# Kernel optimization log

Hardware: AMD Instinct MI355X
Metric: run time of the kernel (lower is better)

Reference implementation:

```python
import jax, jax.numpy as jnp
from jax import lax
import numpy as np

B, S_DEC, S_ENC = 32, 128, 128
V, E, H = 32000, 200, 128


def setup_inputs() -> dict:
    key = jax.random.key(0)
    ks = jax.random.split(key, 10)
    emb = jax.random.normal(ks[0], (V, E), dtype=jnp.float32)
    emb = emb.at[0].set(0.0)  # padding_idx row (char2id[' '] -> 0)
    return {
        "sequence": jax.random.randint(ks[1], (B, S_DEC), 0, V),
        "hs": jax.random.normal(ks[2], (B, S_ENC, H), dtype=jnp.float32),
        "h": jax.random.normal(ks[3], (1, B, H), dtype=jnp.float32),
        "emb": emb,
        "w_ih": jax.random.normal(ks[4], (3 * H, E), dtype=jnp.float32) * 0.05,
        "w_hh": jax.random.normal(ks[5], (3 * H, H), dtype=jnp.float32) * 0.05,
        "b_ih": jax.random.normal(ks[6], (3 * H,), dtype=jnp.float32) * 0.05,
        "b_hh": jax.random.normal(ks[7], (3 * H,), dtype=jnp.float32) * 0.05,
        "w_out": jax.random.normal(ks[8], (V, 2 * H), dtype=jnp.float32) * 0.05,
        "b_out": jax.random.normal(ks[9], (V,), dtype=jnp.float32) * 0.05,
    }


def _gru(x_gates, h0, w_hh, b_hh):
    # x_gates: [B, S, 3H] precomputed input projections; torch gate order r,z,n
    def step(hprev, xg):
        hg = hprev @ w_hh.T + b_hh
        xr, xz, xn = jnp.split(xg, 3, axis=-1)
        hr, hz, hn = jnp.split(hg, 3, axis=-1)
        r = jax.nn.sigmoid(xr + hr)
        z = jax.nn.sigmoid(xz + hz)
        n = jnp.tanh(xn + r * hn)
        hnew = (1.0 - z) * n + z * hprev
        return hnew, hnew

    hT, outs = lax.scan(step, h0, jnp.swapaxes(x_gates, 0, 1))  # scan over time
    return jnp.swapaxes(outs, 0, 1), hT  # [B,S,H], [B,H]


def reference(sequence, hs, h, emb, w_ih, w_hh, b_ih, b_hh, w_out, b_out):
    # Embedding lookup (padding row already zero)
    x = emb[sequence]  # [B, S_dec, E]
    x_gates = jnp.einsum("bse,ge->bsg", x, w_ih) + b_ih  # [B, S_dec, 3H]
    output, hT = _gru(x_gates, h[0], w_hh, b_hh)  # [B, S_dec, H]
    state = hT[None]  # [1, B, H]
    # s = bmm(hs, output^T): [B, S_enc, S_dec]; softmax over encoder axis (dim=1)
    s = jnp.einsum("beh,bdh->bed", hs, output)
    attention_weight = jax.nn.softmax(s, axis=1)
    # context: replaces the per-timestep python loop with one contraction
    c = jnp.einsum("bed,beh->bdh", attention_weight, hs)  # [B, S_dec, H]
    cat = jnp.concatenate([output, c], axis=-1)  # [B, S_dec, 2H]
    logits = jnp.einsum("bdh,vh->bdv", cat, w_out) + b_out  # [B, S_dec, V]
    return logits, state, attention_weight
```

## Files before the change

### kernel.cpp

```cpp
#include <hip/hip_runtime.h>
#include <hip/hip_bf16.h>

#define B_    32
#define SDEC  128
#define SENC  128
#define V_    32000
#define E_    200
#define H_    128
#define G3    384

typedef __attribute__((ext_vector_type(8))) short bf16x8;
typedef __attribute__((ext_vector_type(4))) float f32x4;
typedef __attribute__((ext_vector_type(2))) float f32x2;

#define GLOBAL_AS __attribute__((address_space(1)))
#define LDS_AS    __attribute__((address_space(3)))

__device__ __forceinline__ float fast_sigmoid(float x) {
  return 1.f / (1.f + __expf(-x));
}
__device__ __forceinline__ float fast_tanh(float x) {
  float e2 = __expf(2.f * x);
  return 1.f - 2.f / (e2 + 1.f);
}
__device__ __forceinline__ float quad_reduce(float x) {
  int i = __builtin_bit_cast(int, x);
  int a = __builtin_amdgcn_mov_dpp(i, 0xB1, 0xF, 0xF, true);
  float s = x + __builtin_bit_cast(float, a);
  int j = __builtin_bit_cast(int, s);
  int c = __builtin_amdgcn_mov_dpp(j, 0x4E, 0xF, 0xF, true);
  return s + __builtin_bit_cast(float, c);
}

__global__ __launch_bounds__(192) void k_embed_proj(
    const int* __restrict__ seq, const float* __restrict__ emb,
    const float* __restrict__ w_ih, const float* __restrict__ b_ih,
    float* __restrict__ xg) {
  __shared__ __align__(16) float xs[16][E_];
  __shared__ int sidx[16];
  const int r0 = blockIdx.x * 16;
  const int t = threadIdx.x;
  if (t < 16) sidx[t] = seq[r0 + t];
  __syncthreads();
  for (int i = t; i < 800; i += 192) {
    int r = i / 50, c = i - r * 50;
    *(float4*)&xs[r][c * 4] =
        *(const float4*)(emb + (size_t)sidx[r] * E_ + c * 4);
  }
  __syncthreads();
  const int g0 = t, g1 = t + 192;
  float a0[16], a1[16];
#pragma unroll
  for (int r = 0; r < 16; r++) { a0[r] = 0.f; a1[r] = 0.f; }
  const float* w0 = w_ih + (size_t)g0 * E_;
  const float* w1 = w_ih + (size_t)g1 * E_;
  for (int k = 0; k < E_; k += 4) {
    float4 wv0 = *(const float4*)(w0 + k);
    float4 wv1 = *(const float4*)(w1 + k);
#pragma unroll
    for (int r = 0; r < 16; r++) {
      float4 xv = *(const float4*)&xs[r][k];
      a0[r] += wv0.x * xv.x + wv0.y * xv.y + wv0.z * xv.z + wv0.w * xv.w;
      a1[r] += wv1.x * xv.x + wv1.y * xv.y + wv1.z * xv.z + wv1.w * xv.w;
    }
  }
  const float b0 = b_ih[g0], b1 = b_ih[g1];
#pragma unroll
  for (int r = 0; r < 16; r++) {
    xg[(size_t)(r0 + r) * G3 + g0] = a0[r] + b0;
    xg[(size_t)(r0 + r) * G3 + g1] = a1[r] + b1;
  }
}

__global__ __launch_bounds__(512) void k_gru_attn_cvt(
    const float* __restrict__ xg, const float* __restrict__ h0,
    const float* __restrict__ w_hh, const float* __restrict__ b_hh,
    const float* __restrict__ hs, __hip_bfloat16* __restrict__ cat_bf,
    float* __restrict__ state_out, float* __restrict__ attw_out,
    const float* __restrict__ w_out, __hip_bfloat16* __restrict__ wout_bf) {
  if (blockIdx.x >= 32) {
    const int base = (blockIdx.x - 32) * 4;
#pragma unroll
    for (int j = 0; j < 4; j++) {
      int idx = ((base + j) * 512 + threadIdx.x) * 8;
      float4 a = *(const float4*)(w_out + idx);
      float4 c = *(const float4*)(w_out + idx + 4);
      union { __hip_bfloat16 h[8]; uint4 v; } p;
      p.h[0] = __float2bfloat16(a.x); p.h[1] = __float2bfloat16(a.y);
      p.h[2] = __float2bfloat16(a.z); p.h[3] = __float2bfloat16(a.w);
      p.h[4] = __float2bfloat16(c.x); p.h[5] = __float2bfloat16(c.y);
      p.h[6] = __float2bfloat16(c.z); p.h[7] = __float2bfloat16(c.w);
      *(uint4*)(wout_bf + idx) = p.v;
    }
    return;
  }

  __shared__ __hip_bfloat16 ctb[128][128];
  __shared__ __hip_bfloat16 hsb[128][128];
  __shared__ __hip_bfloat16 hsT[128][128];
  __shared__ __align__(16) float hp[2][H_];

  const int b = blockIdx.x;
  const int t = threadIdx.x;
  const int hh = t >> 2;
  const int sub = t & 3;

  float wr_[32], wz_[32], wn_[32];
#pragma unroll
  for (int m = 0; m < 8; m++) {
    int c = (m + sub * 2) & 7;
    int kb = sub * 32 + c * 4;
    *(float4*)&wr_[m * 4] = *(const float4*)(w_hh + (size_t)hh * H_ + kb);
    *(float4*)&wz_[m * 4] = *(const float4*)(w_hh + (size_t)(128 + hh) * H_ + kb);
    *(float4*)&wn_[m * 4] = *(const float4*)(w_hh + (size_t)(256 + hh) * H_ + kb);
  }

  const float* xgb = xg + (size_t)b * SDEC * G3;
  const float br = b_hh[hh], bz = b_hh[128 + hh], bn = b_hh[256 + hh];
  float cxr = xgb[hh], cxz = xgb[128 + hh], cxn = xgb[256 + hh];
  if (t < H_) hp[0][t] = h0[b * H_ + t];
  __hip_bfloat16* catbfb = cat_bf + (size_t)b * SDEC * 256;

  asm volatile("s_waitcnt lgkmcnt(0)" ::: "memory");
  __builtin_amdgcn_s_barrier();
  asm volatile("" ::: "memory");

  int cur = 0;
  for (int s = 0; s < SDEC; s++) {
    float nxr = 0.f, nxz = 0.f, nxn = 0.f;
    if (s + 1 < SDEC) {
      const float* xp = xgb + (size_t)(s + 1) * G3;
      nxr = xp[hh]; nxz = xp[128 + hh]; nxn = xp[256 + hh];
    }
    f32x2 sr2 = {0.f, 0.f}, sz2 = {0.f, 0.f}, sn2 = {0.f, 0.f};
#pragma unroll
    for (int m = 0; m < 8; m++) {
      int c = (m + sub * 2) & 7;
      float4 hv = *(const float4*)&hp[cur][sub * 32 + c * 4];
      f32x2 h01 = {hv.x, hv.y}, h23 = {hv.z, hv.w};
      const f32x2* w2r = (const f32x2*)&wr_[m * 4];
      const f32x2* w2z = (const f32x2*)&wz_[m * 4];
      const f32x2* w2n = (const f32x2*)&wn_[m * 4];
      sr2 += w2r[0] * h01; sr2 += w2r[1] * h23;
      sz2 += w2z[0] * h01; sz2 += w2z[1] * h23;
      sn2 += w2n[0] * h01; sn2 += w2n[1] * h23;
    }
    float sr = quad_reduce(sr2[0] + sr2[1]);
    float sz = quad_reduce(sz2[0] + sz2[1]);
    float sn = quad_reduce(sn2[0] + sn2[1]);

    float hold = hp[cur][hh];
    float r = fast_sigmoid(cxr + sr + br);
    float z = fast_sigmoid(cxz + sz + bz);
    float n = fast_tanh(cxn + r * (sn + bn));
    float hnew = (1.f - z) * n + z * hold;
    if (sub == 0) {
      __hip_bfloat16 hb = __float2bfloat16(hnew);
      hp[cur ^ 1][hh] = hnew;
      catbfb[(size_t)s * 256 + hh] = hb;
      ctb[s][((hh >> 3) ^ (s & 7)) * 8 + (hh & 7)] = hb;
    }
    asm volatile("s_waitcnt lgkmcnt(0)" ::: "memory");
    __builtin_amdgcn_s_barrier();
    asm volatile("" ::: "memory");
    cur ^= 1;
    cxr = nxr; cxz = nxz; cxn = nxn;
  }

  const int w = t >> 6, l = t & 63;
  const int lr = l & 15, lk = l >> 4;
  const float* hsbase = hs + (size_t)b * SENC * H_;

  for (int i = t; i < 2048; i += 512) {
    int e = i >> 4, c = i & 15;
    float4 v0 = *(const float4*)(hsbase + e * H_ + c * 8);
    float4 v1 = *(const float4*)(hsbase + e * H_ + c * 8 + 4);
    union { __hip_bfloat16 h[8]; uint4 u; } pk;
    pk.h[0] = __float2bfloat16(v0.x); pk.h[1] = __float2bfloat16(v0.y);
    pk.h[2] = __float2bfloat16(v0.z); pk.h[3] = __float2bfloat16(v0.w);
    pk.h[4] = __float2bfloat16(v1.x); pk.h[5] = __float2bfloat16(v1.y);
    pk.h[6] = __float2bfloat16(v1.z); pk.h[7] = __float2bfloat16(v1.w);
    *(uint4*)&hsb[e][((c ^ (e & 7)) * 8)] = pk.u;
  }
  if (t < H_) state_out[b * H_ + t] = hp[cur][t];
  __syncthreads();

  for (int i = t; i < 2048; i += 512) {
    int c = i >> 7, e = i & 127;
    uint4 v = *(const uint4*)&hsb[e][((c ^ (e & 7)) * 8)];
    const __hip_bfloat16* hv = (const __hip_bfloat16*)&v;
#pragma unroll
    for (int u = 0; u < 8; u++) {
      int h = c * 8 + u;
      int col = (e + 8 * (h & 15)) & 127;
      hsT[h][col] = hv[u];
    }
  }
  const int d = w * 16 + lr;
  bf16x8 afrag[4];
#pragma unroll
  for (int kt = 0; kt < 4; kt++)
    afrag[kt] = *(const bf16x8*)&ctb[d][(((kt * 4 + lk) ^ (lr & 7)) * 8)];
  __syncthreads();

  f32x4 acc[8];
#pragma unroll
  for (int et = 0; et < 8; et++) acc[et] = (f32x4){0.f, 0.f, 0.f, 0.f};
#pragma unroll
  for (int et = 0; et < 8; et++) {
#pragma unroll
    for (int kt = 0; kt < 4; kt++) {
      bf16x8 bfrag =
          *(const bf16x8*)&hsb[et * 16 + lr][(((kt * 4 + lk) ^ (lr & 7)) * 8)];
      acc[et] =
          __builtin_amdgcn_mfma_f32_16x16x32_bf16(bfrag, afrag[kt], acc[et], 0, 0, 0);
    }
  }

  float mx = -1e30f;
#pragma unroll
  for (int et = 0; et < 8; et++)
    mx = fmaxf(mx, fmaxf(fmaxf(acc[et][0], acc[et][1]),
                         fmaxf(acc[et][2], acc[et][3])));
  mx = fmaxf(mx, __shfl_xor(mx, 16));
  mx = fmaxf(mx, __shfl_xor(mx, 32));
  float sum = 0.f;
#pragma unroll
  for (int et = 0; et < 8; et++) {
    acc[et][0] = __expf(acc[et][0] - mx);
    acc[et][1] = __expf(acc[et][1] - mx);
    acc[et][2] = __expf(acc[et][2] - mx);
    acc[et][3] = __expf(acc[et][3] - mx);
    sum += acc[et][0] + acc[et][1] + acc[et][2] + acc[et][3];
  }
  sum += __shfl_xor(sum, 16);
  sum += __shfl_xor(sum, 32);
  const float inv = 1.f / sum;

  __hip_bfloat16 (*plds)[128] = ctb;
  float* aw = attw_out + (size_t)b * SENC * SDEC + d;
#pragma unroll
  for (int et = 0; et < 8; et++) {
    acc[et][0] *= inv; acc[et][1] *= inv;
    acc[et][2] *= inv; acc[et][3] *= inv;
    union { __hip_bfloat16 h[4]; uint2 u; } pk4;
    pk4.h[0] = __float2bfloat16(acc[et][0]);
    pk4.h[1] = __float2bfloat16(acc[et][1]);
    pk4.h[2] = __float2bfloat16(acc[et][2]);
    pk4.h[3] = __float2bfloat16(acc[et][3]);
    *(uint2*)&plds[d][(((et * 2 + (lk >> 1)) ^ (lr & 7)) * 8 + 4 * (lk & 1))] =
        pk4.u;
    const int e0 = et * 16 + lk * 4;
#pragma unroll
    for (int j = 0; j < 4; j++)
      aw[(size_t)(e0 + j) * SDEC] = acc[et][j];
  }
  __syncthreads();

  bf16x8 pfrag[4];
#pragma unroll
  for (int f = 0; f < 4; f++)
    pfrag[f] = *(const bf16x8*)&plds[d][(((f * 4 + lk) ^ (lr & 7)) * 8)];
#pragma unroll
  for (int ht = 0; ht < 8; ht++) {
    f32x4 a2 = (f32x4){0.f, 0.f, 0.f, 0.f};
#pragma unroll
    for (int kt = 0; kt < 4; kt++) {
      bf16x8 hfrag =
          *(const bf16x8*)&hsT[ht * 16 + lr][((kt * 32 + lk * 8 + 8 * lr) & 127)];
      a2 = __builtin_amdgcn_mfma_f32_16x16x32_bf16(hfrag, pfrag[kt], a2, 0, 0, 0);
    }
    union { __hip_bfloat16 h[4]; uint2 u; } pk4;
    pk4.h[0] = __float2bfloat16(a2[0]);
    pk4.h[1] = __float2bfloat16(a2[1]);
    pk4.h[2] = __float2bfloat16(a2[2]);
    pk4.h[3] = __float2bfloat16(a2[3]);
    *(uint2*)(cat_bf + (size_t)(b * SDEC + d) * 256 + 128 + ht * 16 + lk * 4) =
        pk4.u;
  }
}

__global__ __launch_bounds__(512) void k_gemm_mfma(
    const __hip_bfloat16* __restrict__ A, const __hip_bfloat16* __restrict__ Bw,
    const float* __restrict__ b_out, float* __restrict__ C) {
  constexpr int K = 256, N = V_, Kt = 32;
  alignas(16) __shared__ char smem[49152];
  __hip_bfloat16 (*As)[4096] = (__hip_bfloat16(*)[4096])smem;
  __hip_bfloat16 (*Bs)[8192] = (__hip_bfloat16(*)[8192])(smem + 16384);
  float* tr = (float*)smem;

  const int tid = threadIdx.x;
  const int w = tid >> 6, l = tid & 63;
  const int wr = w >> 2, wc = w & 3;
  const int lr = l & 15, lk = l >> 4;
  const int lq = l >> 2, lc = l & 3;

  const int bid = blockIdx.x;
  const int wgid = (bid & 7) * 500 + (bid >> 3);
  const int mt = wgid & 31;
  const int nt = wgid >> 5;
  const int m0 = mt * 128, n0 = nt * 256;

  f32x4 acc[4][4];
#pragma unroll
  for (int m = 0; m < 4; m++)
#pragma unroll
    for (int n = 0; n < 4; n++) acc[m][n] = (f32x4){0.f, 0.f, 0.f, 0.f};

#define STAGE(buf, kk)                                                            \
  do {                                                                            \
    const __hip_bfloat16* gA = A + (size_t)(m0 + w * 16 + lq) * K + (kk) + lc * 8;\
    const __hip_bfloat16* gB0 = Bw + (size_t)(n0 + w * 32 + lq) * K + (kk) + lc * 8;\
    const __hip_bfloat16* gB1 = gB0 + (size_t)16 * K;                             \
    __builtin_amdgcn_global_load_lds((const GLOBAL_AS void*)gA,                   \
        (LDS_AS void*)(&As[buf][w * 512]), 16, 0, 0);                             \
    __builtin_amdgcn_global_load_lds((const GLOBAL_AS void*)gB0,                  \
        (LDS_AS void*)(&Bs[buf][w * 1024]), 16, 0, 0);                            \
    __builtin_amdgcn_global_load_lds((const GLOBAL_AS void*)gB1,                  \
        (LDS_AS void*)(&Bs[buf][w * 1024 + 512]), 16, 0, 0);                      \
  } while (0)

  STAGE(0, 0);
  STAGE(1, Kt);

#pragma unroll
  for (int t = 0; t < 8; ++t) {
    if (t < 7) asm volatile("s_waitcnt vmcnt(3)" ::: "memory");
    else       asm volatile("s_waitcnt vmcnt(0)" ::: "memory");
    __builtin_amdgcn_s_barrier();
    asm volatile("" ::: "memory");

    const int c = t & 1;
    bf16x8 af[4], bfr[4];
#pragma unroll
    for (int m = 0; m < 4; m++)
      af[m] = *(const bf16x8*)(const void*)(&As[c][(wr * 64 + m * 16 + lr) * Kt + lk * 8]);
#pragma unroll
    for (int n = 0; n < 4; n++)
      bfr[n] = *(const bf16x8*)(const void*)(&Bs[c][(wc * 64 + n * 16 + lr) * Kt + lk * 8]);

    asm volatile("s_waitcnt lgkmcnt(0)" ::: "memory");
    __builtin_amdgcn_s_barrier();
    asm volatile("" ::: "memory");

    if (t < 6) STAGE(c, (t + 2) * Kt);

    __builtin_amdgcn_s_setprio(1);
#pragma unroll
    for (int m = 0; m < 4; m++)
#pragma unroll
      for (int n = 0; n < 4; n++)
        acc[m][n] = __builtin_amdgcn_mfma_f32_16x16x32_bf16(bfr[n], af[m], acc[m][n], 0, 0, 0);
    __builtin_amdgcn_s_setprio(0);
  }
#undef STAGE

  float4 bo_n[4];
#pragma unroll
  for (int n = 0; n < 4; n++)
    bo_n[n] = *(const float4*)(b_out + n0 + wc * 64 + n * 16 + lk * 4);

  __syncthreads();
#pragma unroll
  for (int q = 0; q < 4; ++q) {
    if (wr == (q >> 1)) {
      const int mbase = 2 * (q & 1);
#pragma unroll
      for (int mm = 0; mm < 2; mm++) {
        const int m = mbase + mm;
        const int row = mm * 16 + lr;
#pragma unroll
        for (int n = 0; n < 4; n++) {
          const int col = wc * 64 + n * 16 + lk * 4;
          f32x4 v;
          v[0] = acc[m][n][0] + bo_n[n].x;
          v[1] = acc[m][n][1] + bo_n[n].y;
          v[2] = acc[m][n][2] + bo_n[n].z;
          v[3] = acc[m][n][3] + bo_n[n].w;
          *(f32x4*)&tr[row * 260 + col] = v;
        }
      }
    }
    __syncthreads();
#pragma unroll
    for (int i = 0; i < 4; ++i) {
      const int c2 = i * 512 + tid;
      const int row = c2 >> 6;
      const int off = (c2 & 63) * 4;
      f32x4 v = *(const f32x4*)&tr[row * 260 + off];
      __builtin_nontemporal_store(
          v, (f32x4*)(C + (size_t)(m0 + q * 32 + row) * N + n0 + off));
    }
    __syncthreads();
  }
}

extern "C" void kernel_launch(void* const* d_in, const int* in_sizes, int n_in,
                              void* d_out, int out_size, void* d_ws, size_t ws_size,
                              hipStream_t stream) {
  const int* seq = (const int*)d_in[0];
  const float* hs = (const float*)d_in[1];
  const float* h0 = (const float*)d_in[2];
  const float* emb = (const float*)d_in[3];
  const float* w_ih = (const float*)d_in[4];
  const float* w_hh = (const float*)d_in[5];
  const float* b_ih = (const float*)d_in[6];
  const float* b_hh = (const float*)d_in[7];
  const float* w_out = (const float*)d_in[8];
  const float* b_out = (const float*)d_in[9];

  float* out = (float*)d_out;
  float* logits = out;
  float* state = out + 131072000;
  float* attw = out + 131072000 + 4096;

  char* ws = (char*)d_ws;
  float* xg = (float*)ws;
  __hip_bfloat16* cat_bf = (__hip_bfloat16*)(ws + 10485760);
  __hip_bfloat16* wout_bf = (__hip_bfloat16*)(ws + 12582912);

  k_embed_proj<<<256, 192, 0, stream>>>(seq, emb, w_ih, b_ih, xg);
  k_gru_attn_cvt<<<532, 512, 0, stream>>>(xg, h0, w_hh, b_hh, hs, cat_bf,
                                          state, attw, w_out, wout_bf);
  k_gemm_mfma<<<4000, 512, 0, stream>>>(cat_bf, wout_bf, b_out, logits);
}
```

Before: 292.3 us.

## Enlarge GEMM M-tile to 256 with triple-buffered LDS and fewer barriers

The logits GEMM now computes 256x256 output tiles per workgroup, so the grid halves and each B tile loaded from global memory is reused across twice as many rows. Staging moves to a three-slot LDS ring, which drops the second per-iteration barrier and the s_setprio hints; A fragments are loaded per m-row inside the MFMA loop. The epilogue writes 64 rows per pass. Separately, the embedding projection kernel uses 128 threads, each computing three gate columns instead of two. The cost is 96KB of LDS and more accumulator registers per workgroup, which limits occupancy to one workgroup per CU.

```diff
diff --git a/kernel.cpp b/kernel.cpp
--- a/kernel.cpp
+++ b/kernel.cpp
@@ -32,7 +32,7 @@
   return s + __builtin_bit_cast(float, c);
 }
 
-__global__ __launch_bounds__(192) void k_embed_proj(
+__global__ __launch_bounds__(128) void k_embed_proj(
     const int* __restrict__ seq, const float* __restrict__ emb,
     const float* __restrict__ w_ih, const float* __restrict__ b_ih,
     float* __restrict__ xg) {
@@ -42,33 +42,37 @@
   const int t = threadIdx.x;
   if (t < 16) sidx[t] = seq[r0 + t];
   __syncthreads();
-  for (int i = t; i < 800; i += 192) {
+  for (int i = t; i < 800; i += 128) {
     int r = i / 50, c = i - r * 50;
     *(float4*)&xs[r][c * 4] =
         *(const float4*)(emb + (size_t)sidx[r] * E_ + c * 4);
   }
   __syncthreads();
-  const int g0 = t, g1 = t + 192;
-  float a0[16], a1[16];
-#pragma unroll
-  for (int r = 0; r < 16; r++) { a0[r] = 0.f; a1[r] = 0.f; }
+  const int g0 = t, g1 = t + 128, g2 = t + 256;
+  float a0[16], a1[16], a2[16];
+#pragma unroll
+  for (int r = 0; r < 16; r++) { a0[r] = 0.f; a1[r] = 0.f; a2[r] = 0.f; }
   const float* w0 = w_ih + (size_t)g0 * E_;
   const float* w1 = w_ih + (size_t)g1 * E_;
+  const float* w2 = w_ih + (size_t)g2 * E_;
   for (int k = 0; k < E_; k += 4) {
     float4 wv0 = *(const float4*)(w0 + k);
     float4 wv1 = *(const float4*)(w1 + k);
+    float4 wv2 = *(const float4*)(w2 + k);
 #pragma unroll
     for (int r = 0; r < 16; r++) {
       float4 xv = *(const float4*)&xs[r][k];
       a0[r] += wv0.x * xv.x + wv0.y * xv.y + wv0.z * xv.z + wv0.w * xv.w;
       a1[r] += wv1.x * xv.x + wv1.y * xv.y + wv1.z * xv.z + wv1.w * xv.w;
-    }
-  }
-  const float b0 = b_ih[g0], b1 = b_ih[g1];
+      a2[r] += wv2.x * xv.x + wv2.y * xv.y + wv2.z * xv.z + wv2.w * xv.w;
+    }
+  }
+  const float b0 = b_ih[g0], b1 = b_ih[g1], b2 = b_ih[g2];
 #pragma unroll
   for (int r = 0; r < 16; r++) {
     xg[(size_t)(r0 + r) * G3 + g0] = a0[r] + b0;
     xg[(size_t)(r0 + r) * G3 + g1] = a1[r] + b1;
+    xg[(size_t)(r0 + r) * G3 + g2] = a2[r] + b2;
   }
 }
 
@@ -280,13 +284,13 @@
   }
 }
 
-__global__ __launch_bounds__(512) void k_gemm_mfma(
+__global__ __launch_bounds__(512, 2) void k_gemm_mfma(
     const __hip_bfloat16* __restrict__ A, const __hip_bfloat16* __restrict__ Bw,
     const float* __restrict__ b_out, float* __restrict__ C) {
   constexpr int K = 256, N = V_, Kt = 32;
-  alignas(16) __shared__ char smem[49152];
-  __hip_bfloat16 (*As)[4096] = (__hip_bfloat16(*)[4096])smem;
-  __hip_bfloat16 (*Bs)[8192] = (__hip_bfloat16(*)[8192])(smem + 16384);
+  alignas(16) __shared__ char smem[98304];
+  __hip_bfloat16 (*As)[8192] = (__hip_bfloat16(*)[8192])smem;
+  __hip_bfloat16 (*Bs)[8192] = (__hip_bfloat16(*)[8192])(smem + 49152);
   float* tr = (float*)smem;
 
   const int tid = threadIdx.x;
@@ -296,24 +300,27 @@
   const int lq = l >> 2, lc = l & 3;
 
   const int bid = blockIdx.x;
-  const int wgid = (bid & 7) * 500 + (bid >> 3);
-  const int mt = wgid & 31;
-  const int nt = wgid >> 5;
-  const int m0 = mt * 128, n0 = nt * 256;
-
-  f32x4 acc[4][4];
-#pragma unroll
-  for (int m = 0; m < 4; m++)
+  const int wgid = (bid & 7) * 250 + (bid >> 3);
+  const int mt = wgid & 15;
+  const int nt = wgid >> 4;
+  const int m0 = mt * 256, n0 = nt * 256;
+
+  f32x4 acc[8][4];
+#pragma unroll
+  for (int m = 0; m < 8; m++)
 #pragma unroll
     for (int n = 0; n < 4; n++) acc[m][n] = (f32x4){0.f, 0.f, 0.f, 0.f};
 
 #define STAGE(buf, kk)                                                            \
   do {                                                                            \
-    const __hip_bfloat16* gA = A + (size_t)(m0 + w * 16 + lq) * K + (kk) + lc * 8;\
+    const __hip_bfloat16* gA0 = A + (size_t)(m0 + w * 32 + lq) * K + (kk) + lc * 8;\
+    const __hip_bfloat16* gA1 = gA0 + (size_t)16 * K;                             \
     const __hip_bfloat16* gB0 = Bw + (size_t)(n0 + w * 32 + lq) * K + (kk) + lc * 8;\
     const __hip_bfloat16* gB1 = gB0 + (size_t)16 * K;                             \
-    __builtin_amdgcn_global_load_lds((const GLOBAL_AS void*)gA,                   \
-        (LDS_AS void*)(&As[buf][w * 512]), 16, 0, 0);                             \
+    __builtin_amdgcn_global_load_lds((const GLOBAL_AS void*)gA0,                  \
+        (LDS_AS void*)(&As[buf][w * 1024]), 16, 0, 0);                            \
+    __builtin_amdgcn_global_load_lds((const GLOBAL_AS void*)gA1,                  \
+        (LDS_AS void*)(&As[buf][w * 1024 + 512]), 16, 0, 0);                      \
     __builtin_amdgcn_global_load_lds((const GLOBAL_AS void*)gB0,                  \
         (LDS_AS void*)(&Bs[buf][w * 1024]), 16, 0, 0);                            \
     __builtin_amdgcn_global_load_lds((const GLOBAL_AS void*)gB1,                  \
@@ -325,33 +332,26 @@
 
 #pragma unroll
   for (int t = 0; t < 8; ++t) {
-    if (t < 7) asm volatile("s_waitcnt vmcnt(3)" ::: "memory");
+    if (t < 7) asm volatile("s_waitcnt vmcnt(4)" ::: "memory");
     else       asm volatile("s_waitcnt vmcnt(0)" ::: "memory");
     __builtin_amdgcn_s_barrier();
     asm volatile("" ::: "memory");
 
-    const int c = t & 1;
-    bf16x8 af[4], bfr[4];
-#pragma unroll
-    for (int m = 0; m < 4; m++)
-      af[m] = *(const bf16x8*)(const void*)(&As[c][(wr * 64 + m * 16 + lr) * Kt + lk * 8]);
+    const int c = t % 3;
+    bf16x8 bfr[4];
 #pragma unroll
     for (int n = 0; n < 4; n++)
       bfr[n] = *(const bf16x8*)(const void*)(&Bs[c][(wc * 64 + n * 16 + lr) * Kt + lk * 8]);
 
-    asm volatile("s_waitcnt lgkmcnt(0)" ::: "memory");
-    __builtin_amdgcn_s_barrier();
-    asm volatile("" ::: "memory");
-
-    if (t < 6) STAGE(c, (t + 2) * Kt);
-
-    __builtin_amdgcn_s_setprio(1);
-#pragma unroll
-    for (int m = 0; m < 4; m++)
+    if (t < 6) STAGE((t + 2) % 3, (t + 2) * Kt);
+
+#pragma unroll
+    for (int m = 0; m < 8; m++) {
+      bf16x8 af = *(const bf16x8*)(const void*)(&As[c][(wr * 128 + m * 16 + lr) * Kt + lk * 8]);
 #pragma unroll
       for (int n = 0; n < 4; n++)
-        acc[m][n] = __builtin_amdgcn_mfma_f32_16x16x32_bf16(bfr[n], af[m], acc[m][n], 0, 0, 0);
-    __builtin_amdgcn_s_setprio(0);
+        acc[m][n] = __builtin_amdgcn_mfma_f32_16x16x32_bf16(bfr[n], af, acc[m][n], 0, 0, 0);
+    }
   }
 #undef STAGE
 
@@ -364,9 +364,9 @@
 #pragma unroll
   for (int q = 0; q < 4; ++q) {
     if (wr == (q >> 1)) {
-      const int mbase = 2 * (q & 1);
-#pragma unroll
-      for (int mm = 0; mm < 2; mm++) {
+      const int mbase = (q & 1) * 4;
+#pragma unroll
+      for (int mm = 0; mm < 4; mm++) {
         const int m = mbase + mm;
         const int row = mm * 16 + lr;
 #pragma unroll
@@ -383,13 +383,13 @@
     }
     __syncthreads();
 #pragma unroll
-    for (int i = 0; i < 4; ++i) {
+    for (int i = 0; i < 8; ++i) {
       const int c2 = i * 512 + tid;
       const int row = c2 >> 6;
       const int off = (c2 & 63) * 4;
       f32x4 v = *(const f32x4*)&tr[row * 260 + off];
       __builtin_nontemporal_store(
-          v, (f32x4*)(C + (size_t)(m0 + q * 32 + row) * N + n0 + off));
+          v, (f32x4*)(C + (size_t)(m0 + q * 64 + row) * N + n0 + off));
     }
     __syncthreads();
   }
@@ -419,8 +419,8 @@
   __hip_bfloat16* cat_bf = (__hip_bfloat16*)(ws + 10485760);
   __hip_bfloat16* wout_bf = (__hip_bfloat16*)(ws + 12582912);
 
-  k_embed_proj<<<256, 192, 0, stream>>>(seq, emb, w_ih, b_ih, xg);
+  k_embed_proj<<<256, 128, 0, stream>>>(seq, emb, w_ih, b_ih, xg);
   k_gru_attn_cvt<<<532, 512, 0, stream>>>(xg, h0, w_hh, b_hh, hs, cat_bf,
                                           state, attw, w_out, wout_bf);
-  k_gemm_mfma<<<4000, 512, 0, stream>>>(cat_bf, wout_bf, b_out, logits);
-}
+  k_gemm_mfma<<<2000, 512, 0, stream>>>(cat_bf, wout_bf, b_out, logits);
+}
```

After: 307.4 us. 5.2% more time.
